# Performance work log

Measured on AMD Instinct MI355X. Metric: run time of the kernel, lower is better.

The kernel has to match this reference:

```python
import jax, jax.numpy as jnp
from jax import lax
import numpy as np

B, T, D, H, K = 16, 2048, 512, 512, 2

def setup_inputs() -> dict:
    key = jax.random.key(0)
    k1, k2, k3 = jax.random.split(key, 3)
    inputs = jax.random.normal(k1, (B, T, D), dtype=jnp.float32)
    conv_w = jax.random.normal(k2, (3 * H, D, K), dtype=jnp.float32) * (1.0 / np.sqrt(D * K))
    conv_b = jax.random.normal(k3, (3 * H,), dtype=jnp.float32) * 0.01
    return {"inputs": inputs, "conv_w": conv_w, "conv_b": conv_b}

def reference(inputs, conv_w, conv_b):
    # inputs: [B, T, D]; conv_w: [3H, D, K]; causal conv via left-pad K-1
    k = conv_w.shape[-1]
    h = conv_w.shape[0] // 3
    x = jnp.transpose(inputs, (0, 2, 1))                      # [B, D, T]
    x = jnp.pad(x, ((0, 0), (0, 0), (k - 1, 0)))              # left pad
    gates = lax.conv_general_dilated(
        x, conv_w, window_strides=(1,), padding='VALID',
        dimension_numbers=('NCH', 'OIH', 'NCH'))              # [B, 3H, T]
    gates = jnp.transpose(gates, (0, 2, 1)) + conv_b          # [B, T, 3H]
    Z, F, O = jnp.split(gates, 3, axis=2)
    Z = jnp.tanh(Z)
    F = jax.nn.sigmoid(F)
    O = jax.nn.sigmoid(O)

    # fo-pool: c_t = f_t * c_{t-1} + (1 - f_t) * z_t, c_{-1} = 0
    def step(c, zf):
        z, f = zf
        c_ = f * c + (1.0 - f) * z
        return c_, c_

    c0 = jnp.zeros((Z.shape[0], h), dtype=Z.dtype)
    _, C = lax.scan(step, c0, (jnp.swapaxes(Z, 0, 1), jnp.swapaxes(F, 0, 1)))
    C = jnp.swapaxes(C, 0, 1)                                 # [B, T, H]
    return C, O * C
```

## Files before the change

### kernel.cpp

```cpp
#include <hip/hip_runtime.h>


#define MTOT 32768
#define NTOT 1536
#define KTOT 1024
#define DCH  512
#define TLEN 2048
#define NB   16

#define LC2    64
#define NCH    32
#define CHAINS 8192

#define GBK 32
#define NKT (KTOT / GBK)

typedef __bf16 bf16x8 __attribute__((ext_vector_type(8)));
typedef float  f32x4  __attribute__((ext_vector_type(4)));

__device__ __forceinline__ unsigned short f2bf(float x) {
    unsigned u = __float_as_uint(x);
    u += 0x7FFFu + ((u >> 16) & 1u);
    return (unsigned short)(u >> 16);
}
__device__ __forceinline__ float bf2f(unsigned short h) {
    return __uint_as_float(((unsigned)h) << 16);
}
__device__ __forceinline__ float sigmoidf_(float x) {
    return 1.f / (1.f + __expf(-x));
}

__global__ __launch_bounds__(256) void make_A(const float* __restrict__ in,
                                              unsigned short* __restrict__ A) {
    size_t i = (size_t)blockIdx.x * 256 + threadIdx.x;
    size_t e = i * 8;
    size_t m = e >> 10;
    int    j = (int)(e & 1023);
    alignas(16) unsigned short h[8];
    if (((m & (TLEN - 1)) == 0) && (j < DCH)) {
#pragma unroll
        for (int r = 0; r < 8; ++r) h[r] = 0;
    } else {
        const float* src = in + ((long long)m - 1) * DCH + j;
        float4 a = *(const float4*)src;
        float4 b = *(const float4*)(src + 4);
        h[0] = f2bf(a.x); h[1] = f2bf(a.y); h[2] = f2bf(a.z); h[3] = f2bf(a.w);
        h[4] = f2bf(b.x); h[5] = f2bf(b.y); h[6] = f2bf(b.z); h[7] = f2bf(b.w);
    }
    *(int4*)(A + e) = *(const int4*)h;
}

__global__ __launch_bounds__(256) void make_B(const float* __restrict__ w,
                                              unsigned short* __restrict__ Bt) {
    int i = blockIdx.x * 256 + threadIdx.x;
    int o = i >> 9, d = i & 511;
    float w0 = w[(size_t)(o * 512 + d) * 2];
    float w1 = w[(size_t)(o * 512 + d) * 2 + 1];
    Bt[(size_t)o * 1024 + d]       = f2bf(w0);
    Bt[(size_t)o * 1024 + 512 + d] = f2bf(w1);
}

__global__ __launch_bounds__(512) void gemm_gates(const unsigned short* __restrict__ A,
                                                  const unsigned short* __restrict__ B,
                                                  const float* __restrict__ bias,
                                                  unsigned short* __restrict__ GT) {
    __shared__ int4 lds4[8192];

    const int tid = threadIdx.x;
    const int bx0 = blockIdx.x;
    const int bx  = (bx0 & 7) * 96 + (bx0 >> 3);
    const int mT  = bx / 6, nT = bx % 6;
    const int m0  = mT * 256, n0 = nT * 256;

    const int r0 = tid >> 2, q = tid & 3;
    const int qs = q ^ ((r0 >> 1) & 3);
    const unsigned short* ga0 = A + (size_t)(m0 + r0) * 1024 + qs * 8;
    const unsigned short* ga1 = A + (size_t)(m0 + 128 + r0) * 1024 + qs * 8;
    const unsigned short* gb0 = B + (size_t)(n0 + r0) * 1024 + qs * 8;
    const unsigned short* gb1 = B + (size_t)(n0 + 128 + r0) * 1024 + qs * 8;
    char* ldsc = (char*)lds4;

    const int lane = tid & 63;
    const int wv   = tid >> 6;
    const int wm   = wv >> 2, wn = wv & 3;
    const int lr   = lane & 15, lq = lane >> 4;

    int aidx[2][4], bidx[4];
#pragma unroll
    for (int h = 0; h < 2; ++h)
#pragma unroll
        for (int i = 0; i < 4; ++i) {
            int row = wm * 128 + h * 64 + i * 16 + lr;
            aidx[h][i] = row * 4 + (lq ^ ((row >> 1) & 3));
        }
#pragma unroll
    for (int j = 0; j < 4; ++j) {
        int col = wn * 64 + j * 16 + lr;
        bidx[j] = 1024 + col * 4 + (lq ^ ((col >> 1) & 3));
    }

    f32x4 acc[8][4] = {};

#define GLL(SRC, DOFF) __builtin_amdgcn_global_load_lds( \
        (__attribute__((address_space(1))) void*)(void*)(SRC), \
        (__attribute__((address_space(3))) void*)(ldsc + (DOFF)), 16, 0, 0)

#define STAGE_A(U) { const int bb_ = ((U) & 3) * 32768; \
        GLL(ga0 + (size_t)(U) * GBK, bb_ + tid * 16); \
        GLL(ga1 + (size_t)(U) * GBK, bb_ + 8192 + tid * 16); }
#define STAGE_B(U) { const int bb_ = ((U) & 3) * 32768; \
        GLL(gb0 + (size_t)(U) * GBK, bb_ + 16384 + tid * 16); \
        GLL(gb1 + (size_t)(U) * GBK, bb_ + 24576 + tid * 16); }

    STAGE_A(0); STAGE_B(0);
    STAGE_A(1); STAGE_B(1);
    STAGE_A(2); STAGE_B(2);

#define TILE(T, VW, DO_STAGE) { \
        asm volatile("s_waitcnt vmcnt(" VW ")" ::: "memory"); \
        __builtin_amdgcn_s_barrier(); \
        __builtin_amdgcn_sched_barrier(0); \
        const int bufo = ((T) & 3) * 2048; \
        bf16x8 bf[4], af[4]; \
        _Pragma("unroll") \
        for (int j = 0; j < 4; ++j) bf[j] = __builtin_bit_cast(bf16x8, lds4[bufo + bidx[j]]); \
        _Pragma("unroll") \
        for (int i = 0; i < 4; ++i) af[i] = __builtin_bit_cast(bf16x8, lds4[bufo + aidx[0][i]]); \
        if (DO_STAGE) STAGE_A((T) + 3); \
        __builtin_amdgcn_s_setprio(1); \
        _Pragma("unroll") \
        for (int i = 0; i < 4; ++i) \
            _Pragma("unroll") \
            for (int j = 0; j < 4; ++j) \
                acc[i][j] = __builtin_amdgcn_mfma_f32_16x16x32_bf16(af[i], bf[j], acc[i][j], 0, 0, 0); \
        __builtin_amdgcn_s_setprio(0); \
        _Pragma("unroll") \
        for (int i = 0; i < 4; ++i) af[i] = __builtin_bit_cast(bf16x8, lds4[bufo + aidx[1][i]]); \
        if (DO_STAGE) STAGE_B((T) + 3); \
        __builtin_amdgcn_s_setprio(1); \
        _Pragma("unroll") \
        for (int i = 0; i < 4; ++i) \
            _Pragma("unroll") \
            for (int j = 0; j < 4; ++j) \
                acc[4 + i][j] = __builtin_amdgcn_mfma_f32_16x16x32_bf16(af[i], bf[j], acc[4 + i][j], 0, 0, 0); \
        __builtin_amdgcn_s_setprio(0); }

    for (int t = 0; t < NKT - 3; ++t)
        TILE(t, "8", 1);
    TILE(NKT - 3, "8", 0);
    TILE(NKT - 2, "4", 0);
    TILE(NKT - 1, "0", 0);

#undef TILE
#undef STAGE_A
#undef STAGE_B
#undef GLL

#pragma unroll
    for (int j = 0; j < 4; ++j) {
        int gn = n0 + wn * 64 + j * 16 + lr;
        float bj = bias[gn];
#pragma unroll
        for (int i = 0; i < 8; ++i) {
            int gm = m0 + wm * 128 + i * 16 + lq * 4;
            alignas(8) unsigned short pk[4];
#pragma unroll
            for (int r = 0; r < 4; ++r) pk[r] = f2bf(acc[i][j][r] + bj);
            *(int2*)(GT + (size_t)gn * MTOT + gm) = *(const int2*)pk;
        }
    }
}

__global__ __launch_bounds__(256) void scan_part1(const unsigned short* __restrict__ GT,
                                                  float* __restrict__ Pws,
                                                  float* __restrict__ Cws) {
    const int tid   = threadIdx.x;
    const int h_loc = tid & 31;
    const int sc    = tid >> 5;
    const int bid   = blockIdx.x;
    const int tg    = bid & 3;
    const int hg    = (bid >> 2) & 15;
    const int b     = bid >> 6;
    const int h     = hg * 32 + h_loc;
    const int cg    = tg * 8 + sc;

    const size_t mbase = (size_t)b * TLEN + (size_t)cg * LC2;
    const unsigned short* gz = GT + (size_t)h * MTOT + mbase;
    const unsigned short* gf = GT + (size_t)(DCH + h) * MTOT + mbase;

    bf16x8 zv[8], fv[8];
#pragma unroll
    for (int q = 0; q < 8; ++q) zv[q] = *(const bf16x8*)(gz + q * 8);
#pragma unroll
    for (int q = 0; q < 8; ++q) fv[q] = *(const bf16x8*)(gf + q * 8);

    float P = 1.f, c = 0.f;
#pragma unroll
    for (int q = 0; q < 8; ++q)
#pragma unroll
        for (int r = 0; r < 8; ++r) {
            float f = sigmoidf_((float)fv[q][r]);
            float z = 2.f * sigmoidf_(2.f * (float)zv[q][r]) - 1.f;
            c = f * c + (1.f - f) * z;
            P *= f;
        }
    const int ch = b * DCH + h;
    Pws[(size_t)cg * CHAINS + ch] = P;
    Cws[(size_t)cg * CHAINS + ch] = c;
}

__global__ __launch_bounds__(256) void scan_part2(const float* __restrict__ Pws,
                                                  const float* __restrict__ Cws,
                                                  float* __restrict__ Iws) {
    const int ch = blockIdx.x * 256 + threadIdx.x;
    float Pv[NCH], Cv[NCH];
#pragma unroll
    for (int cg = 0; cg < NCH; ++cg) Pv[cg] = Pws[(size_t)cg * CHAINS + ch];
#pragma unroll
    for (int cg = 0; cg < NCH; ++cg) Cv[cg] = Cws[(size_t)cg * CHAINS + ch];
    float cc = 0.f;
#pragma unroll
    for (int cg = 0; cg < NCH; ++cg) {
        Iws[(size_t)cg * CHAINS + ch] = cc;
        cc = Pv[cg] * cc + Cv[cg];
    }
}

__global__ __launch_bounds__(256) void scan_part3(const unsigned short* __restrict__ GT,
                                                  const float* __restrict__ Iws,
                                                  float* __restrict__ out) {
    const int tid   = threadIdx.x;
    const int h_loc = tid & 31;
    const int sc    = tid >> 5;
    const int bid   = blockIdx.x;
    const int tg    = bid & 3;
    const int hg    = (bid >> 2) & 15;
    const int b     = bid >> 6;
    const int h     = hg * 32 + h_loc;
    const int cg    = tg * 8 + sc;

    const size_t mbase = (size_t)b * TLEN + (size_t)cg * LC2;
    const unsigned short* gz = GT + (size_t)h * MTOT + mbase;
    const unsigned short* gf = GT + (size_t)(DCH + h) * MTOT + mbase;
    const unsigned short* go = GT + (size_t)(2 * DCH + h) * MTOT + mbase;

    bf16x8 zv[8], fv[8], ov[8];
#pragma unroll
    for (int q = 0; q < 8; ++q) zv[q] = *(const bf16x8*)(gz + q * 8);
#pragma unroll
    for (int q = 0; q < 8; ++q) fv[q] = *(const bf16x8*)(gf + q * 8);
#pragma unroll
    for (int q = 0; q < 8; ++q) ov[q] = *(const bf16x8*)(go + q * 8);

    const int ch = b * DCH + h;
    float c = Iws[(size_t)cg * CHAINS + ch];

    const size_t BTH = (size_t)NB * TLEN * DCH;
    float* oC  = out + mbase * DCH + h;
    float* oOC = oC + BTH;
#pragma unroll
    for (int q = 0; q < 8; ++q)
#pragma unroll
        for (int r = 0; r < 8; ++r) {
            float f = sigmoidf_((float)fv[q][r]);
            float z = 2.f * sigmoidf_(2.f * (float)zv[q][r]) - 1.f;
            float o = sigmoidf_((float)ov[q][r]);
            c = f * c + (1.f - f) * z;
            __builtin_nontemporal_store(c,     oC  + (size_t)(q * 8 + r) * DCH);
            __builtin_nontemporal_store(o * c, oOC + (size_t)(q * 8 + r) * DCH);
        }
}

extern "C" void kernel_launch(void* const* d_in, const int* in_sizes, int n_in,
                              void* d_out, int out_size, void* d_ws, size_t ws_size,
                              hipStream_t stream) {
    const float* in   = (const float*)d_in[0];
    const float* w    = (const float*)d_in[1];
    const float* bias = (const float*)d_in[2];
    float* out = (float*)d_out;

    unsigned short* Abf = (unsigned short*)d_ws;
    unsigned short* Bbf = Abf + (size_t)MTOT * 1024;
    unsigned short* GT  = Bbf + (size_t)NTOT * 1024;

    float* Pws = (float*)d_ws;
    float* Cws = Pws + (size_t)NCH * CHAINS;
    float* Iws = Cws + (size_t)NCH * CHAINS;

    make_A<<<dim3(16384), dim3(256), 0, stream>>>(in, Abf);
    make_B<<<dim3(3072),  dim3(256), 0, stream>>>(w, Bbf);
    gemm_gates<<<dim3(768), dim3(512), 0, stream>>>(Abf, Bbf, bias, GT);
    scan_part1<<<dim3(1024), dim3(256), 0, stream>>>(GT, Pws, Cws);
    scan_part2<<<dim3(CHAINS / 256), dim3(256), 0, stream>>>(Pws, Cws, Iws);
    scan_part3<<<dim3(1024), dim3(256), 0, stream>>>(GT, Iws, out);
}
```

Before: 400.4 us.

## Halve GEMM LDS pipeline depth for occupancy and shorten scan chunks

The gate GEMM drops from a 4-stage to a 2-stage LDS ring buffer, halving shared memory per block. It now issues both A and B prefetches for the next tile at the start of each tile and waits on vmcnt(0). It also adds a min-blocks-per-CU launch bound of 4, aiming for more resident blocks per CU. The chunked scan uses 64 chunks of 32 timesteps instead of 32 of 64, doubling blocks in the first and third scan kernels, and scan_part2 processes prefixes in blocks of 16. The risks are lost memory/compute overlap in the GEMM and register pressure or spills from the tighter launch bound, given the large accumulator array.

```diff
diff --git a/kernel.cpp b/kernel.cpp
--- a/kernel.cpp
+++ b/kernel.cpp
@@ -8,8 +8,8 @@
 #define TLEN 2048
 #define NB   16
 
-#define LC2    64
-#define NCH    32
+#define LC2    32
+#define NCH    64
 #define CHAINS 8192
 
 #define GBK 32
@@ -60,11 +60,11 @@
     Bt[(size_t)o * 1024 + 512 + d] = f2bf(w1);
 }
 
-__global__ __launch_bounds__(512) void gemm_gates(const unsigned short* __restrict__ A,
-                                                  const unsigned short* __restrict__ B,
-                                                  const float* __restrict__ bias,
-                                                  unsigned short* __restrict__ GT) {
-    __shared__ int4 lds4[8192];
+__global__ __launch_bounds__(512, 4) void gemm_gates(const unsigned short* __restrict__ A,
+                                                     const unsigned short* __restrict__ B,
+                                                     const float* __restrict__ bias,
+                                                     unsigned short* __restrict__ GT) {
+    __shared__ int4 lds4[4096];
 
     const int tid = threadIdx.x;
     const int bx0 = blockIdx.x;
@@ -105,28 +105,26 @@
         (__attribute__((address_space(1))) void*)(void*)(SRC), \
         (__attribute__((address_space(3))) void*)(ldsc + (DOFF)), 16, 0, 0)
 
-#define STAGE_A(U) { const int bb_ = ((U) & 3) * 32768; \
+#define STAGE_A(U) { const int bb_ = ((U) & 1) * 32768; \
         GLL(ga0 + (size_t)(U) * GBK, bb_ + tid * 16); \
         GLL(ga1 + (size_t)(U) * GBK, bb_ + 8192 + tid * 16); }
-#define STAGE_B(U) { const int bb_ = ((U) & 3) * 32768; \
+#define STAGE_B(U) { const int bb_ = ((U) & 1) * 32768; \
         GLL(gb0 + (size_t)(U) * GBK, bb_ + 16384 + tid * 16); \
         GLL(gb1 + (size_t)(U) * GBK, bb_ + 24576 + tid * 16); }
 
     STAGE_A(0); STAGE_B(0);
-    STAGE_A(1); STAGE_B(1);
-    STAGE_A(2); STAGE_B(2);
-
-#define TILE(T, VW, DO_STAGE) { \
-        asm volatile("s_waitcnt vmcnt(" VW ")" ::: "memory"); \
+
+#define TILE(T, DO_STAGE) { \
+        asm volatile("s_waitcnt vmcnt(0)" ::: "memory"); \
         __builtin_amdgcn_s_barrier(); \
         __builtin_amdgcn_sched_barrier(0); \
-        const int bufo = ((T) & 3) * 2048; \
+        const int bufo = ((T) & 1) * 2048; \
+        if (DO_STAGE) { STAGE_A((T) + 1); STAGE_B((T) + 1); } \
         bf16x8 bf[4], af[4]; \
         _Pragma("unroll") \
         for (int j = 0; j < 4; ++j) bf[j] = __builtin_bit_cast(bf16x8, lds4[bufo + bidx[j]]); \
         _Pragma("unroll") \
         for (int i = 0; i < 4; ++i) af[i] = __builtin_bit_cast(bf16x8, lds4[bufo + aidx[0][i]]); \
-        if (DO_STAGE) STAGE_A((T) + 3); \
         __builtin_amdgcn_s_setprio(1); \
         _Pragma("unroll") \
         for (int i = 0; i < 4; ++i) \
@@ -136,7 +134,6 @@
         __builtin_amdgcn_s_setprio(0); \
         _Pragma("unroll") \
         for (int i = 0; i < 4; ++i) af[i] = __builtin_bit_cast(bf16x8, lds4[bufo + aidx[1][i]]); \
-        if (DO_STAGE) STAGE_B((T) + 3); \
         __builtin_amdgcn_s_setprio(1); \
         _Pragma("unroll") \
         for (int i = 0; i < 4; ++i) \
@@ -145,11 +142,9 @@
                 acc[4 + i][j] = __builtin_amdgcn_mfma_f32_16x16x32_bf16(af[i], bf[j], acc[4 + i][j], 0, 0, 0); \
         __builtin_amdgcn_s_setprio(0); }
 
-    for (int t = 0; t < NKT - 3; ++t)
-        TILE(t, "8", 1);
-    TILE(NKT - 3, "8", 0);
-    TILE(NKT - 2, "4", 0);
-    TILE(NKT - 1, "0", 0);
+    for (int t = 0; t < NKT - 1; ++t)
+        TILE(t, 1);
+    TILE(NKT - 1, 0);
 
 #undef TILE
 #undef STAGE_A
@@ -178,9 +173,9 @@
     const int h_loc = tid & 31;
     const int sc    = tid >> 5;
     const int bid   = blockIdx.x;
-    const int tg    = bid & 3;
-    const int hg    = (bid >> 2) & 15;
-    const int b     = bid >> 6;
+    const int tg    = bid & 7;
+    const int hg    = (bid >> 3) & 15;
+    const int b     = bid >> 7;
     const int h     = hg * 32 + h_loc;
     const int cg    = tg * 8 + sc;
 
@@ -188,15 +183,15 @@
     const unsigned short* gz = GT + (size_t)h * MTOT + mbase;
     const unsigned short* gf = GT + (size_t)(DCH + h) * MTOT + mbase;
 
-    bf16x8 zv[8], fv[8];
-#pragma unroll
-    for (int q = 0; q < 8; ++q) zv[q] = *(const bf16x8*)(gz + q * 8);
-#pragma unroll
-    for (int q = 0; q < 8; ++q) fv[q] = *(const bf16x8*)(gf + q * 8);
+    bf16x8 zv[4], fv[4];
+#pragma unroll
+    for (int q = 0; q < 4; ++q) zv[q] = *(const bf16x8*)(gz + q * 8);
+#pragma unroll
+    for (int q = 0; q < 4; ++q) fv[q] = *(const bf16x8*)(gf + q * 8);
 
     float P = 1.f, c = 0.f;
 #pragma unroll
-    for (int q = 0; q < 8; ++q)
+    for (int q = 0; q < 4; ++q)
 #pragma unroll
         for (int r = 0; r < 8; ++r) {
             float f = sigmoidf_((float)fv[q][r]);
@@ -213,16 +208,18 @@
                                                   const float* __restrict__ Cws,
                                                   float* __restrict__ Iws) {
     const int ch = blockIdx.x * 256 + threadIdx.x;
-    float Pv[NCH], Cv[NCH];
-#pragma unroll
-    for (int cg = 0; cg < NCH; ++cg) Pv[cg] = Pws[(size_t)cg * CHAINS + ch];
-#pragma unroll
-    for (int cg = 0; cg < NCH; ++cg) Cv[cg] = Cws[(size_t)cg * CHAINS + ch];
     float cc = 0.f;
-#pragma unroll
-    for (int cg = 0; cg < NCH; ++cg) {
-        Iws[(size_t)cg * CHAINS + ch] = cc;
-        cc = Pv[cg] * cc + Cv[cg];
+    for (int blk = 0; blk < NCH / 16; ++blk) {
+        float Pv[16], Cv[16];
+#pragma unroll
+        for (int i = 0; i < 16; ++i) Pv[i] = Pws[(size_t)(blk * 16 + i) * CHAINS + ch];
+#pragma unroll
+        for (int i = 0; i < 16; ++i) Cv[i] = Cws[(size_t)(blk * 16 + i) * CHAINS + ch];
+#pragma unroll
+        for (int i = 0; i < 16; ++i) {
+            Iws[(size_t)(blk * 16 + i) * CHAINS + ch] = cc;
+            cc = Pv[i] * cc + Cv[i];
+        }
     }
 }
 
@@ -233,9 +230,9 @@
     const int h_loc = tid & 31;
     const int sc    = tid >> 5;
     const int bid   = blockIdx.x;
-    const int tg    = bid & 3;
-    const int hg    = (bid >> 2) & 15;
-    const int b     = bid >> 6;
+    const int tg    = bid & 7;
+    const int hg    = (bid >> 3) & 15;
+    const int b     = bid >> 7;
     const int h     = hg * 32 + h_loc;
     const int cg    = tg * 8 + sc;
 
@@ -244,13 +241,13 @@
     const unsigned short* gf = GT + (size_t)(DCH + h) * MTOT + mbase;
     const unsigned short* go = GT + (size_t)(2 * DCH + h) * MTOT + mbase;
 
-    bf16x8 zv[8], fv[8], ov[8];
-#pragma unroll
-    for (int q = 0; q < 8; ++q) zv[q] = *(const bf16x8*)(gz + q * 8);
-#pragma unroll
-    for (int q = 0; q < 8; ++q) fv[q] = *(const bf16x8*)(gf + q * 8);
-#pragma unroll
-    for (int q = 0; q < 8; ++q) ov[q] = *(const bf16x8*)(go + q * 8);
+    bf16x8 zv[4], fv[4], ov[4];
+#pragma unroll
+    for (int q = 0; q < 4; ++q) zv[q] = *(const bf16x8*)(gz + q * 8);
+#pragma unroll
+    for (int q = 0; q < 4; ++q) fv[q] = *(const bf16x8*)(gf + q * 8);
+#pragma unroll
+    for (int q = 0; q < 4; ++q) ov[q] = *(const bf16x8*)(go + q * 8);
 
     const int ch = b * DCH + h;
     float c = Iws[(size_t)cg * CHAINS + ch];
@@ -259,7 +256,7 @@
     float* oC  = out + mbase * DCH + h;
     float* oOC = oC + BTH;
 #pragma unroll
-    for (int q = 0; q < 8; ++q)
+    for (int q = 0; q < 4; ++q)
 #pragma unroll
         for (int r = 0; r < 8; ++r) {
             float f = sigmoidf_((float)fv[q][r]);
@@ -290,7 +287,7 @@
     make_A<<<dim3(16384), dim3(256), 0, stream>>>(in, Abf);
     make_B<<<dim3(3072),  dim3(256), 0, stream>>>(w, Bbf);
     gemm_gates<<<dim3(768), dim3(512), 0, stream>>>(Abf, Bbf, bias, GT);
-    scan_part1<<<dim3(1024), dim3(256), 0, stream>>>(GT, Pws, Cws);
+    scan_part1<<<dim3(2048), dim3(256), 0, stream>>>(GT, Pws, Cws);
     scan_part2<<<dim3(CHAINS / 256), dim3(256), 0, stream>>>(Pws, Cws, Iws);
-    scan_part3<<<dim3(1024), dim3(256), 0, stream>>>(GT, Iws, out);
-}
+    scan_part3<<<dim3(2048), dim3(256), 0, stream>>>(GT, Iws, out);
+}
```

Measured after the change: 1.255 ms. +213.4%, slower.
